# Kernel tuning notes

Measured on AMD Instinct MI355X. Metric: run time of the kernel, lower is better.

The kernel has to match this reference:

```python
import jax, jax.numpy as jnp
import numpy as np
from jax import lax

N_CLASS = 21
K_ED = 5
ALPHA = 0.1
BN_EPS = 1e-5


def _conv(x, w):
    # NCHW conv, stride 1, SAME padding
    return lax.conv_general_dilated(x, w, (1, 1), 'SAME',
                                    dimension_numbers=('NCHW', 'OIHW', 'NCHW'))


def _bn(x, g, b, m, v):
    # inference-mode BatchNorm2d with running stats
    scale = (g * lax.rsqrt(v + BN_EPS))[None, :, None, None]
    return (x - m[None, :, None, None]) * scale + b[None, :, None, None]


def _maxpool(x, k):
    return lax.reduce_window(x, -jnp.inf, lax.max, (1, 1, k, k), (1, 1, 1, 1), 'SAME')


def setup_inputs() -> dict:
    key = jax.random.key(0)
    ks = jax.random.split(key, 12)
    N, F, H, W, C = 8, 512, 96, 96, N_CLASS
    feature = jax.random.normal(ks[0], (N, F, H, W), jnp.float32)
    global_pred = jax.random.normal(ks[1], (N, C, H, W), jnp.float32)
    conv1_w = jax.random.normal(ks[2], (256, F, 3, 3), jnp.float32) * 0.02
    bn1_g = jnp.ones((256,), jnp.float32)
    bn1_b = jnp.zeros((256,), jnp.float32)
    bn1_m = jax.random.normal(ks[3], (256,), jnp.float32) * 0.1
    bn1_v = jax.random.uniform(ks[4], (256,), jnp.float32, 0.5, 1.5)
    conv2_w = jax.random.normal(ks[5], (128, 256, 3, 3), jnp.float32) * 0.02
    bn2_g = jnp.ones((128,), jnp.float32)
    bn2_b = jnp.zeros((128,), jnp.float32)
    bn2_m = jax.random.normal(ks[6], (128,), jnp.float32) * 0.1
    bn2_v = jax.random.uniform(ks[7], (128,), jnp.float32, 0.5, 1.5)
    conv3_w = jax.random.normal(ks[8], (C, 128, 1, 1), jnp.float32) * 0.02
    conv3_b = jnp.zeros((C,), jnp.float32)
    return dict(feature=feature, global_pred=global_pred,
                conv1_w=conv1_w, bn1_g=bn1_g, bn1_b=bn1_b, bn1_m=bn1_m, bn1_v=bn1_v,
                conv2_w=conv2_w, bn2_g=bn2_g, bn2_b=bn2_b, bn2_m=bn2_m, bn2_v=bn2_v,
                conv3_w=conv3_w, conv3_b=conv3_b)


def reference(feature, global_pred, conv1_w, bn1_g, bn1_b, bn1_m, bn1_v,
              conv2_w, bn2_g, bn2_b, bn2_m, bn2_v, conv3_w, conv3_b):
    N, F, H, W = feature.shape
    # hard labels -> one-hot [N, C, H, W]
    lbl = jnp.argmax(global_pred, axis=1)
    onehot = jnp.transpose(jax.nn.one_hot(lbl, N_CLASS, dtype=feature.dtype), (0, 3, 1, 2))
    # binary morphology: dilation = max-pool, erosion = -max-pool(-x)
    d = _maxpool(onehot, K_ED)
    e = -_maxpool(-onehot, K_ED)
    transition = jnp.sum(d - e, axis=1, keepdims=True)
    transition = jnp.where(transition >= 1.0, 1.0, transition)  # [N,1,H,W]
    tfeat = feature * transition
    # per-class masked mean over ALL H*W pixels (faithful to .mean(dim=2))
    objs = jnp.einsum('nfhw,nchw->ncf', feature, e) / (H * W)  # [N,C,F]
    # cdist(p=2) between transition-feature pixels and class prototypes
    x = tfeat.reshape(N, F, H * W).transpose(0, 2, 1)  # [N,HW,F]
    x2 = jnp.sum(x * x, axis=-1, keepdims=True)
    o2 = jnp.sum(objs * objs, axis=-1)
    d2 = jnp.maximum(x2 + o2[:, None, :] - 2.0 * jnp.einsum('npf,ncf->npc', x, objs), 0.0)
    cd = jnp.where(d2 > 0, jnp.sqrt(jnp.where(d2 > 0, d2, 1.0)), 0.0)  # safe sqrt
    dist = 1.0 - jax.nn.softmax(cd, axis=-1)  # [N,HW,C]
    obj_feat = jnp.einsum('npc,ncf->nfp', dist, objs).reshape(N, F, H, W)
    fusion = (feature * (1.0 - transition)
              + feature * transition * ALPHA
              + obj_feat * transition * (1.0 - ALPHA))
    # fusion_predictor: convBNReLU -> bilinear x2 -> convBNReLU -> 1x1 conv
    h = jax.nn.relu(_bn(_conv(fusion, conv1_w), bn1_g, bn1_b, bn1_m, bn1_v))
    h = jax.image.resize(h, (N, 256, 2 * H, 2 * W), method='bilinear')
    h = jax.nn.relu(_bn(_conv(h, conv2_w), bn2_g, bn2_b, bn2_m, bn2_v))
    logits = _conv(h, conv3_w) + conv3_b[None, :, None, None]
    # eval mode: softmax over classes
    return jax.nn.softmax(logits, axis=1)
```

## Files before the change

### kernel.cpp

```cpp
#include <hip/hip_runtime.h>
#include <cstdint>
#include <cstddef>

typedef __attribute__((ext_vector_type(4))) float f32x4;
typedef __attribute__((ext_vector_type(8))) short short8;

__device__ __forceinline__ float bf2f(unsigned short u) {
  union { unsigned int i; float f; } x; x.i = ((unsigned int)u) << 16; return x.f;
}
__device__ __forceinline__ unsigned short f2bf(float f) {
  union { float f; unsigned int i; } x; x.f = f;
  unsigned int r = x.i + 0x7fffu + ((x.i >> 16) & 1u);
  return (unsigned short)(r >> 16);
}
__device__ __forceinline__ void gload16(unsigned short* lds, const unsigned short* g) {
  __builtin_amdgcn_global_load_lds(
      (const __attribute__((address_space(1))) unsigned int*)g,
      (__attribute__((address_space(3))) unsigned int*)lds, 16, 0, 0);
}

__global__ void k_prepbn(const float* __restrict__ g1, const float* __restrict__ b1,
                         const float* __restrict__ m1, const float* __restrict__ v1,
                         const float* __restrict__ g2, const float* __restrict__ b2,
                         const float* __restrict__ m2, const float* __restrict__ v2,
                         float* __restrict__ s1, float* __restrict__ bb1,
                         float* __restrict__ s2, float* __restrict__ bb2) {
  int i = threadIdx.x;
  if (i < 256) { float s = g1[i] * rsqrtf(v1[i] + 1e-5f); s1[i] = s; bb1[i] = b1[i] - m1[i] * s; }
  if (i < 128) { float s = g2[i] * rsqrtf(v2[i] + 1e-5f); s2[i] = s; bb2[i] = b2[i] - m2[i] * s; }
}

__global__ void k_prepw1(const float* __restrict__ w, unsigned short* __restrict__ wt) {
  int i = blockIdx.x * 256 + threadIdx.x;
  int o = i / 4608, k = i - o * 4608;
  int cblk = k / 288, r = k - cblk * 288;
  int t = r >> 5, cl = r & 31;
  int ci = cblk * 32 + cl;
  int ty = t / 3, tx = t - ty * 3;
  wt[i] = f2bf(w[((o * 512 + ci) * 3 + ty) * 3 + tx]);
}
__global__ void k_prepw2(const float* __restrict__ w, unsigned short* __restrict__ wt) {
  int i = blockIdx.x * 256 + threadIdx.x;
  int o = i / 2304, k = i - o * 2304;
  int cblk = k / 288, r = k - cblk * 288;
  int t = r >> 5, cl = r & 31;
  int ci = cblk * 32 + cl;
  int ty = t / 3, tx = t - ty * 3;
  wt[i] = f2bf(w[((o * 256 + ci) * 3 + ty) * 3 + tx]);
}
__global__ void k_prepw3(const float* __restrict__ w3, unsigned short* __restrict__ w3b) {
  int i = blockIdx.x * 256 + threadIdx.x;
  int c = i >> 7, k = i & 127;
  w3b[i] = (c < 21) ? f2bf(w3[c * 128 + k]) : (unsigned short)0;
}

template <int HP, int WP, int C>
__global__ void k_border(unsigned short* __restrict__ p) {
  const int B = 2 * WP + 2 * (HP - 2);
  const int total = 8 * B * (C / 8);
  int i = blockIdx.x * 256 + threadIdx.x;
  if (i >= total) return;
  const int cg = i % (C / 8);
  int b = i / (C / 8);
  const int n = b / B; b -= n * B;
  int y, x;
  if (b < WP) { y = 0; x = b; }
  else if (b < 2 * WP) { y = HP - 1; x = b - WP; }
  else { int r = b - 2 * WP; y = 1 + (r >> 1); x = (r & 1) ? (WP - 1) : 0; }
  short8 z = {0, 0, 0, 0, 0, 0, 0, 0};
  *(short8*)&p[(((long)n * HP + y) * WP + x) * C + cg * 8] = z;
}

__global__ __launch_bounds__(256)
void k_featT(const float* __restrict__ feat, unsigned short* __restrict__ featT) {
  const int g = blockIdx.x * 256 + threadIdx.x;
  const int n = g / 9216, p = g - n * 9216;
  const int fg0 = blockIdx.y * 16;
  const float* src = feat + (long)n * 512 * 9216 + p;
  unsigned short* dst = featT + ((long)n * 9216 + p) * 512;
  for (int fg = fg0; fg < fg0 + 16; fg++) {
    short8 o;
    #pragma unroll
    for (int j = 0; j < 8; j++) o[j] = (short)f2bf(src[(long)(fg * 8 + j) * 9216]);
    *(short8*)&dst[fg * 8] = o;
  }
}

__global__ void k_labels(const float* __restrict__ gp, signed char* __restrict__ lab) {
  int p = blockIdx.x * 256 + threadIdx.x;
  int n = p / 9216, q = p - n * 9216;
  const float* g = gp + (long)n * 21 * 9216 + q;
  float best = g[0]; int bi = 0;
  #pragma unroll
  for (int c = 1; c < 21; c++) {
    float v = g[(long)c * 9216];
    if (v > best) { best = v; bi = c; }
  }
  lab[p] = (signed char)bi;
}

__global__ void k_em(const signed char* __restrict__ lab, signed char* __restrict__ em) {
  int p = blockIdx.x * 256 + threadIdx.x;
  int n = p / 9216, q = p - n * 9216, y = q / 96, x = q - y * 96;
  const signed char* L = lab + n * 9216;
  signed char l0 = L[q];
  bool uni = true;
  for (int dy = -2; dy <= 2; dy++) {
    int yy = y + dy; if (yy < 0 || yy > 95) continue;
    for (int dx = -2; dx <= 2; dx++) {
      int xx = x + dx; if (xx < 0 || xx > 95) continue;
      uni = uni && (L[yy * 96 + xx] == l0);
    }
  }
  em[p] = uni ? l0 : (signed char)-1;
}

__global__ __launch_bounds__(256)
void k_objsT(const unsigned short* __restrict__ featT, const signed char* __restrict__ em,
             float* __restrict__ objs) {
  __shared__ float part[21 * 512];
  __shared__ signed char emL[256];
  __shared__ int pres[21];
  const int b = blockIdx.x;
  const int n = b / 36;
  const int px0 = (b - n * 36) * 256;
  const int tid = threadIdx.x;
  for (int i = tid; i < 21 * 512; i += 256) part[i] = 0.f;
  if (tid < 21) pres[tid] = 0;
  emL[tid] = em[n * 9216 + px0 + tid];
  __syncthreads();
  const unsigned short* base = featT + ((long)n * 9216 + px0) * 512 + tid * 2;
  for (int px = 0; px < 256; px++) {
    const int c0 = emL[px];
    if (c0 >= 0) {
      if (tid == 0) pres[c0] = 1;
      unsigned int v = *(const unsigned int*)&base[(long)px * 512];
      atomicAdd(&part[c0 * 512 + tid * 2], bf2f((unsigned short)(v & 0xffff)));
      atomicAdd(&part[c0 * 512 + tid * 2 + 1], bf2f((unsigned short)(v >> 16)));
    }
  }
  __syncthreads();
  for (int i = tid; i < 21 * 512; i += 256) {
    const int c = i >> 9;
    if (pres[c]) atomicAdd(&objs[(long)n * 21 * 512 + i], part[i] * (1.0f / 9216.0f));
  }
}

__global__ void k_o2(const float* __restrict__ objs, float* __restrict__ o2) {
  int nc = blockIdx.x;
  int lane = threadIdx.x;
  const float* o = objs + (long)nc * 512;
  float s = 0.f;
  for (int f = lane; f < 512; f += 64) { float v = o[f]; s += v * v; }
  #pragma unroll
  for (int off = 32; off; off >>= 1) s += __shfl_down(s, off);
  if (lane == 0) o2[nc] = s;
}

__global__ void k_objsbf(const float* __restrict__ objs, unsigned short* __restrict__ oc) {
  int i = blockIdx.x * 256 + threadIdx.x;
  int n = i / (32 * 512); int r = i - n * 32 * 512;
  int c = r >> 9, f = r & 511;
  oc[i] = (c < 21) ? f2bf(objs[((long)n * 21 + c) * 512 + f]) : (unsigned short)0;
}

__global__ __launch_bounds__(256)
void k_dist_mfma(const unsigned short* __restrict__ featT,
                 const unsigned short* __restrict__ objs_c,
                 const float* __restrict__ o2, float* __restrict__ dist) {
  const int n = blockIdx.y;
  const int w = threadIdx.x >> 6, lane = threadIdx.x & 63;
  const int lrow = lane & 15, kg = lane >> 4;
  const int px = blockIdx.x * 64 + w * 16 + lrow;
  const unsigned short* fb = featT + ((long)n * 9216 + px) * 512 + kg * 8;
  const unsigned short* a0p = objs_c + ((long)n * 32 + lrow) * 512 + kg * 8;
  const unsigned short* a1p = a0p + 16 * 512;
  f32x4 acc0 = {0.f, 0.f, 0.f, 0.f}, acc1 = {0.f, 0.f, 0.f, 0.f};
  float x2 = 0.f;
  #pragma unroll
  for (int s = 0; s < 16; s++) {
    const short8 b = *(const short8*)&fb[s * 32];
    const short8 a0 = *(const short8*)&a0p[s * 32];
    const short8 a1 = *(const short8*)&a1p[s * 32];
    acc0 = __builtin_amdgcn_mfma_f32_16x16x32_bf16(a0, b, acc0, 0, 0, 0);
    acc1 = __builtin_amdgcn_mfma_f32_16x16x32_bf16(a1, b, acc1, 0, 0, 0);
    #pragma unroll
    for (int j = 0; j < 8; j++) { float v = bf2f((unsigned short)b[j]); x2 += v * v; }
  }
  x2 += __shfl_xor(x2, 16); x2 += __shfl_xor(x2, 32);
  float cd[8], mx = -1e30f;
  #pragma unroll
  for (int r = 0; r < 4; r++) {
    const int c = kg * 4 + r;
    float d2 = x2 + o2[n * 21 + c] - 2.f * acc0[r];
    cd[r] = sqrtf(fmaxf(d2, 0.f)); mx = fmaxf(mx, cd[r]);
  }
  #pragma unroll
  for (int r = 0; r < 4; r++) {
    const int c = 16 + kg * 4 + r;
    if (c < 21) {
      float d2 = x2 + o2[n * 21 + c] - 2.f * acc1[r];
      cd[4 + r] = sqrtf(fmaxf(d2, 0.f)); mx = fmaxf(mx, cd[4 + r]);
    } else cd[4 + r] = -1e30f;
  }
  mx = fmaxf(mx, __shfl_xor(mx, 16)); mx = fmaxf(mx, __shfl_xor(mx, 32));
  float sum = 0.f;
  #pragma unroll
  for (int k = 0; k < 8; k++) {
    cd[k] = (cd[k] > -1e29f) ? __expf(cd[k] - mx) : 0.f;
    sum += cd[k];
  }
  sum += __shfl_xor(sum, 16); sum += __shfl_xor(sum, 32);
  const float inv = 1.f / sum;
  #pragma unroll
  for (int r = 0; r < 4; r++)
    dist[((long)n * 21 + kg * 4 + r) * 9216 + px] = 1.f - cd[r] * inv;
  #pragma unroll
  for (int r = 0; r < 4; r++) {
    const int c = 16 + kg * 4 + r;
    if (c < 21) dist[((long)n * 21 + c) * 9216 + px] = 1.f - cd[4 + r] * inv;
  }
}

__global__ __launch_bounds__(256)
void k_fusion(const unsigned short* __restrict__ featT, const signed char* __restrict__ em,
              const float* __restrict__ dist, const float* __restrict__ objs,
              unsigned short* __restrict__ fuP) {
  __shared__ float ob[21 * 512];
  __shared__ float dl[64][21];
  __shared__ signed char eml[64];
  const int blk = blockIdx.x;
  const int n = blk / 144;
  const int p0 = (blk - n * 144) * 64;
  const int tid = threadIdx.x;
  for (int i = tid; i < 21 * 512; i += 256) ob[i] = objs[(long)n * 21 * 512 + i];
  for (int i = tid; i < 64 * 21; i += 256) {
    int px = i & 63, c = i >> 6;
    dl[px][c] = dist[((long)n * 21 + c) * 9216 + p0 + px];
  }
  if (tid < 64) eml[tid] = em[n * 9216 + p0 + tid];
  __syncthreads();
  const int px = tid & 63;
  const int fg = (tid >> 6) * 8;
  const int q = p0 + px;
  const int y = q / 96, x = q - y * 96;
  unsigned short* dst = fuP + (((long)n * 98 + y + 1) * 98 + (x + 1)) * 512;
  const bool t = eml[px] < 0;
  const unsigned short* srcT = featT + ((long)n * 9216 + q) * 512;
  for (int f0 = 0; f0 < 512; f0 += 32) {
    short8 o;
    const short8 fvv = *(const short8*)&srcT[f0 + fg];
    #pragma unroll
    for (int j = 0; j < 8; j++) {
      const int f = f0 + fg + j;
      float fv = bf2f((unsigned short)fvv[j]);
      if (t) {
        float of = 0.f;
        #pragma unroll
        for (int c = 0; c < 21; c++) of += dl[px][c] * ob[c * 512 + f];
        fv = 0.1f * fv + 0.9f * of;
      }
      o[j] = (short)f2bf(fv);
    }
    *(short8*)&dst[fg] = o;
    dst += 32;
  }
}

template <int CIN, int NK>
__global__ __launch_bounds__(256)
void conv3x3_gemm(const unsigned short* __restrict__ inP,
                  const unsigned short* __restrict__ wT,
                  const float* __restrict__ scale, const float* __restrict__ bias,
                  unsigned short* __restrict__ out,
                  int Hout, int Wout, int Hp, int Wp, int COUT, int nbN) {
  __shared__ unsigned short ldsA[3][4096];
  __shared__ unsigned short ldsB[3][4096];
  const int tid = threadIdx.x;
  const int chunk = gridDim.x >> 3;
  const int bid = (blockIdx.x & 7) * chunk + (blockIdx.x >> 3);
  const int mb = bid / nbN, nb = bid - mb * nbN;
  const int bm0 = mb * 128, bn0 = nb * 128;
  const int KT = 9 * CIN;
  const int HWo = Hout * Wout;

  const int rA = tid >> 2;
  const int ch8 = (((tid & 3) ^ ((tid >> 3) & 3)) * 8);
  const int m0 = bm0 + rA, m1 = m0 + 64;
  const int n0 = m0 / HWo; const int q0 = m0 - n0 * HWo;
  const int y0 = q0 / Wout, x0 = q0 - y0 * Wout;
  const int n1 = m1 / HWo; const int q1 = m1 - n1 * HWo;
  const int y1 = q1 / Wout, x1 = q1 - y1 * Wout;
  const unsigned short* gA0 = inP + ((long)(n0 * Hp + y0) * Wp + x0) * CIN + ch8;
  const unsigned short* gA1 = inP + ((long)(n1 * Hp + y1) * Wp + x1) * CIN + ch8;
  const unsigned short* gB0 = wT + (long)(bn0 + rA) * KT + ch8;
  const unsigned short* gB1 = wT + (long)(bn0 + rA + 64) * KT + ch8;

  const int lane = tid & 63;
  const int wv = tid >> 6;
  const int wr = wv >> 1, wc = wv & 1;
  const int lrow = lane & 15, kg = lane >> 4;
  const int arow = wr * 64 + lrow;
  const int aoff = arow * 32 + (kg ^ ((arow >> 1) & 3)) * 8;
  const int brow = wc * 64 + lrow;
  const int boff = brow * 32 + (kg ^ ((brow >> 1) & 3)) * 8;

  f32x4 acc[4][4];
  const f32x4 zero = {0.f, 0.f, 0.f, 0.f};
  #pragma unroll
  for (int i = 0; i < 4; i++)
    #pragma unroll
    for (int j = 0; j < 4; j++) acc[i][j] = zero;

  auto stage = [&](int b, int s) {
    const int cblk = s / 9;
    const int t = s - cblk * 9;
    const int ty = t / 3, tx = t - ty * 3;
    const long offA = (long)(ty * Wp + tx) * CIN + cblk * 32;
    gload16(&ldsA[b][tid * 8], gA0 + offA);
    gload16(&ldsA[b][2048 + tid * 8], gA1 + offA);
    const long k0 = (long)s * 32;
    gload16(&ldsB[b][tid * 8], gB0 + k0);
    gload16(&ldsB[b][2048 + tid * 8], gB1 + k0);
  };

  auto kstep = [&](int rd) {
    const unsigned short* A = ldsA[rd];
    const unsigned short* B = ldsB[rd];
    short8 af[4], bfr[4];
    #pragma unroll
    for (int i = 0; i < 4; i++) af[i] = *(const short8*)&A[aoff + i * 512];
    #pragma unroll
    for (int j = 0; j < 4; j++) bfr[j] = *(const short8*)&B[boff + j * 512];
    __builtin_amdgcn_s_setprio(1);
    #pragma unroll
    for (int i = 0; i < 4; i++)
      #pragma unroll
      for (int j = 0; j < 4; j++)
        acc[i][j] = __builtin_amdgcn_mfma_f32_16x16x32_bf16(af[i], bfr[j], acc[i][j], 0, 0, 0);
    __builtin_amdgcn_s_setprio(0);
  };

  stage(0, 0);
  stage(1, 1);
  int rd = 0;
  for (int s = 0; s < NK; ++s) {
    if (s < NK - 1)
      asm volatile("s_waitcnt vmcnt(6)" ::: "memory");
    else
      asm volatile("s_waitcnt vmcnt(0)" ::: "memory");
    __builtin_amdgcn_s_barrier();
    asm volatile("" ::: "memory");
    kstep(rd);
    if (s + 2 < NK) stage((rd + 2 >= 3) ? rd - 1 : rd + 2, s + 2);
    rd = (rd == 2) ? 0 : rd + 1;
  }

  #pragma unroll
  for (int i = 0; i < 4; i++) {
    const int row = bm0 + wr * 64 + i * 16 + kg * 4;
    #pragma unroll
    for (int j = 0; j < 4; j++) {
      const int col = bn0 + wc * 64 + j * 16 + lrow;
      const float sc = scale[col], bi = bias[col];
      #pragma unroll
      for (int r = 0; r < 4; r++) {
        float v = acc[i][j][r] * sc + bi;
        v = v > 0.f ? v : 0.f;
        out[(long)(row + r) * COUT + col] = f2bf(v);
      }
    }
  }
}

__global__ void k_upsample(const unsigned short* __restrict__ h1,
                           unsigned short* __restrict__ h2P) {
  const int idx = blockIdx.x * 256 + threadIdx.x;
  const int c8 = (idx & 31) * 8;
  const int p = idx >> 5;
  const int n = p / 36864; const int rr = p - n * 36864;
  const int Y = rr / 192, X = rr - Y * 192;
  const int ky = Y >> 1, kx = X >> 1;
  int yA, yB, xA, xB; float wyA, wyB, wxA, wxB;
  if ((Y & 1) == 0) { yA = ky > 0 ? ky - 1 : 0; yB = ky; wyA = 0.25f; wyB = 0.75f; }
  else { yA = ky; yB = ky < 95 ? ky + 1 : 95; wyA = 0.75f; wyB = 0.25f; }
  if ((X & 1) == 0) { xA = kx > 0 ? kx - 1 : 0; xB = kx; wxA = 0.25f; wxB = 0.75f; }
  else { xA = kx; xB = kx < 95 ? kx + 1 : 95; wxA = 0.75f; wxB = 0.25f; }
  const unsigned short* hb = h1 + (long)n * 96 * 96 * 256 + c8;
  const short8 vaa = *(const short8*)&hb[((long)yA * 96 + xA) * 256];
  const short8 vab = *(const short8*)&hb[((long)yA * 96 + xB) * 256];
  const short8 vba = *(const short8*)&hb[((long)yB * 96 + xA) * 256];
  const short8 vbb = *(const short8*)&hb[((long)yB * 96 + xB) * 256];
  short8 o;
  #pragma unroll
  for (int j = 0; j < 8; j++) {
    float v = wyA * (wxA * bf2f((unsigned short)vaa[j]) + wxB * bf2f((unsigned short)vab[j])) +
              wyB * (wxA * bf2f((unsigned short)vba[j]) + wxB * bf2f((unsigned short)vbb[j]));
    o[j] = (short)f2bf(v);
  }
  *(short8*)&h2P[(((long)n * 194 + Y + 1) * 194 + X + 1) * 256 + c8] = o;
}

__global__ __launch_bounds__(256)
void k_conv3_mfma(const unsigned short* __restrict__ h3,
                  const unsigned short* __restrict__ w3b,
                  const float* __restrict__ b3, float* __restrict__ out) {
  const int w = threadIdx.x >> 6, lane = threadIdx.x & 63;
  const int lrow = lane & 15, kg = lane >> 4;
  const long m = (long)blockIdx.x * 64 + w * 16 + lrow;
  const unsigned short* bp = h3 + m * 128 + kg * 8;
  const unsigned short* a0p = w3b + lrow * 128 + kg * 8;
  const unsigned short* a1p = a0p + 16 * 128;
  f32x4 acc0 = {0.f, 0.f, 0.f, 0.f}, acc1 = {0.f, 0.f, 0.f, 0.f};
  #pragma unroll
  for (int s = 0; s < 4; s++) {
    const short8 b = *(const short8*)&bp[s * 32];
    const short8 a0 = *(const short8*)&a0p[s * 32];
    const short8 a1 = *(const short8*)&a1p[s * 32];
    acc0 = __builtin_amdgcn_mfma_f32_16x16x32_bf16(a0, b, acc0, 0, 0, 0);
    acc1 = __builtin_amdgcn_mfma_f32_16x16x32_bf16(a1, b, acc1, 0, 0, 0);
  }
  float lg[8], mx = -1e30f;
  #pragma unroll
  for (int r = 0; r < 4; r++) {
    lg[r] = acc0[r] + b3[kg * 4 + r];
    mx = fmaxf(mx, lg[r]);
  }
  #pragma unroll
  for (int r = 0; r < 4; r++) {
    const int c = 16 + kg * 4 + r;
    if (c < 21) { lg[4 + r] = acc1[r] + b3[c]; mx = fmaxf(mx, lg[4 + r]); }
    else lg[4 + r] = -1e30f;
  }
  mx = fmaxf(mx, __shfl_xor(mx, 16)); mx = fmaxf(mx, __shfl_xor(mx, 32));
  float sum = 0.f;
  #pragma unroll
  for (int k = 0; k < 8; k++) {
    lg[k] = (lg[k] > -1e29f) ? __expf(lg[k] - mx) : 0.f;
    sum += lg[k];
  }
  sum += __shfl_xor(sum, 16); sum += __shfl_xor(sum, 32);
  const float inv = 1.f / sum;
  const int n = (int)(m / 36864);
  const int q = (int)(m - (long)n * 36864);
  #pragma unroll
  for (int r = 0; r < 4; r++)
    out[((long)n * 21 + kg * 4 + r) * 36864 + q] = lg[r] * inv;
  #pragma unroll
  for (int r = 0; r < 4; r++) {
    const int c = 16 + kg * 4 + r;
    if (c < 21) out[((long)n * 21 + c) * 36864 + q] = lg[4 + r] * inv;
  }
}

extern "C" void kernel_launch(void* const* d_in, const int* in_sizes, int n_in,
                              void* d_out, int out_size, void* d_ws, size_t ws_size,
                              hipStream_t stream) {
  const float* feature = (const float*)d_in[0];
  const float* gp = (const float*)d_in[1];
  const float* w1 = (const float*)d_in[2];
  const float* g1 = (const float*)d_in[3];
  const float* b1 = (const float*)d_in[4];
  const float* m1 = (const float*)d_in[5];
  const float* v1 = (const float*)d_in[6];
  const float* w2 = (const float*)d_in[7];
  const float* g2 = (const float*)d_in[8];
  const float* b2 = (const float*)d_in[9];
  const float* m2 = (const float*)d_in[10];
  const float* v2 = (const float*)d_in[11];
  const float* w3 = (const float*)d_in[12];
  const float* b3 = (const float*)d_in[13];
  float* out = (float*)d_out;

  char* ws = (char*)d_ws;
  size_t off = 0;
  auto alloc = [&](size_t bytes) -> void* {
    void* p = ws + off;
    off += (bytes + 255) & ~(size_t)255;
    return p;
  };
  signed char* lab = (signed char*)alloc(73728);
  signed char* em = (signed char*)alloc(73728);
  float* objs = (float*)alloc(8 * 21 * 512 * 4);
  float* o2 = (float*)alloc(168 * 4);
  unsigned short* objs_c = (unsigned short*)alloc((size_t)8 * 32 * 512 * 2);
  float* dist = (float*)alloc((size_t)8 * 21 * 9216 * 4);
  unsigned short* w1t = (unsigned short*)alloc((size_t)256 * 4608 * 2);
  unsigned short* w2t = (unsigned short*)alloc((size_t)128 * 2304 * 2);
  unsigned short* w3b = (unsigned short*)alloc((size_t)32 * 128 * 2);
  float* s1 = (float*)alloc(256 * 4);
  float* bb1 = (float*)alloc(256 * 4);
  float* s2 = (float*)alloc(128 * 4);
  float* bb2 = (float*)alloc(128 * 4);
  const size_t fuP_bytes = (size_t)8 * 98 * 98 * 512 * 2;
  unsigned short* fuP = (unsigned short*)alloc(fuP_bytes);
  const size_t h1_bytes = (size_t)8 * 96 * 96 * 256 * 2;
  unsigned short* h1 = (unsigned short*)alloc(h1_bytes);
  const size_t h2P_bytes = (size_t)8 * 194 * 194 * 256 * 2;
  unsigned short* h2P = (unsigned short*)alloc(h2P_bytes);
  unsigned short* h3 = fuP;
  unsigned short* featT = h2P;

  if (off > ws_size) return;

  k_prepbn<<<1, 256, 0, stream>>>(g1, b1, m1, v1, g2, b2, m2, v2, s1, bb1, s2, bb2);
  k_prepw1<<<4608, 256, 0, stream>>>(w1, w1t);
  k_prepw2<<<1152, 256, 0, stream>>>(w2, w2t);
  k_prepw3<<<16, 256, 0, stream>>>(w3, w3b);

  k_border<98, 98, 512><<<777, 256, 0, stream>>>(fuP);
  hipMemsetAsync(objs, 0, 8 * 21 * 512 * 4, stream);

  k_labels<<<288, 256, 0, stream>>>(gp, lab);
  k_em<<<288, 256, 0, stream>>>(lab, em);
  k_featT<<<dim3(288, 4), 256, 0, stream>>>(feature, featT);
  k_objsT<<<288, 256, 0, stream>>>(featT, em, objs);
  k_o2<<<168, 64, 0, stream>>>(objs, o2);
  k_objsbf<<<512, 256, 0, stream>>>(objs, objs_c);
  k_dist_mfma<<<dim3(144, 8), 256, 0, stream>>>(featT, objs_c, o2, dist);
  k_fusion<<<1152, 256, 0, stream>>>(featT, em, dist, objs, fuP);

  conv3x3_gemm<512, 144><<<1152, 256, 0, stream>>>(fuP, w1t, s1, bb1, h1,
                                                   96, 96, 98, 98, 256, 2);
  k_border<194, 194, 256><<<772, 256, 0, stream>>>(h2P);
  k_upsample<<<36864, 256, 0, stream>>>(h1, h2P);
  conv3x3_gemm<256, 72><<<2304, 256, 0, stream>>>(h2P, w2t, s2, bb2, h3,
                                                  192, 192, 194, 194, 128, 1);
  k_conv3_mfma<<<4608, 256, 0, stream>>>(h3, w3b, b3, out);
}
```

Before: 796.5 us.

## Fuse conv2 with 1x1 conv3 and softmax; deepen conv1 pipeline to 4 stages

The second 3x3 conv GEMM now keeps its BN+ReLU output tile in shared memory and immediately applies the 1x1 classifier conv via MFMA plus softmax. This removes the h3 intermediate write/read and a separate kernel launch. Separately, the generic conv GEMM (now used only for conv1) moves from triple to quadruple LDS buffering, with three stages in flight and adjusted vmcnt waits. The deeper buffering raises LDS use per block and may reduce occupancy.

```diff
diff --git a/kernel.cpp b/kernel.cpp
--- a/kernel.cpp
+++ b/kernel.cpp
@@ -274,8 +274,8 @@
                   const float* __restrict__ scale, const float* __restrict__ bias,
                   unsigned short* __restrict__ out,
                   int Hout, int Wout, int Hp, int Wp, int COUT, int nbN) {
-  __shared__ unsigned short ldsA[3][4096];
-  __shared__ unsigned short ldsB[3][4096];
+  __shared__ unsigned short ldsA[4][4096];
+  __shared__ unsigned short ldsB[4][4096];
   const int tid = threadIdx.x;
   const int chunk = gridDim.x >> 3;
   const int bid = (blockIdx.x & 7) * chunk + (blockIdx.x >> 3);
@@ -343,17 +343,18 @@
 
   stage(0, 0);
   stage(1, 1);
-  int rd = 0;
+  stage(2, 2);
   for (int s = 0; s < NK; ++s) {
-    if (s < NK - 1)
-      asm volatile("s_waitcnt vmcnt(6)" ::: "memory");
+    if (s <= NK - 3)
+      asm volatile("s_waitcnt vmcnt(8)" ::: "memory");
+    else if (s == NK - 2)
+      asm volatile("s_waitcnt vmcnt(4)" ::: "memory");
     else
       asm volatile("s_waitcnt vmcnt(0)" ::: "memory");
     __builtin_amdgcn_s_barrier();
     asm volatile("" ::: "memory");
-    kstep(rd);
-    if (s + 2 < NK) stage((rd + 2 >= 3) ? rd - 1 : rd + 2, s + 2);
-    rd = (rd == 2) ? 0 : rd + 1;
+    kstep(s & 3);
+    if (s + 3 < NK) stage((s + 3) & 3, s + 3);
   }
 
   #pragma unroll
@@ -369,6 +370,165 @@
         v = v > 0.f ? v : 0.f;
         out[(long)(row + r) * COUT + col] = f2bf(v);
       }
+    }
+  }
+}
+
+__global__ __launch_bounds__(256)
+void conv2_fused(const unsigned short* __restrict__ inP,
+                 const unsigned short* __restrict__ wT,
+                 const float* __restrict__ scale, const float* __restrict__ bias,
+                 const unsigned short* __restrict__ w3b, const float* __restrict__ b3,
+                 float* __restrict__ out) {
+  constexpr int CIN = 256, NK = 72;
+  constexpr int Wout = 192, Hp = 194, Wp = 194;
+  constexpr int HWo = 192 * 192;
+  constexpr int KT = 9 * CIN;
+  __shared__ unsigned short pool[6 * 4096];
+  const int tid = threadIdx.x;
+  const int chunk = gridDim.x >> 3;
+  const int bid = (blockIdx.x & 7) * chunk + (blockIdx.x >> 3);
+  const int bm0 = bid * 128;
+
+  const int rA = tid >> 2;
+  const int ch8 = (((tid & 3) ^ ((tid >> 3) & 3)) * 8);
+  const int m0 = bm0 + rA, m1 = m0 + 64;
+  const int n0 = m0 / HWo; const int q0 = m0 - n0 * HWo;
+  const int y0 = q0 / Wout, x0 = q0 - y0 * Wout;
+  const int n1 = m1 / HWo; const int q1 = m1 - n1 * HWo;
+  const int y1 = q1 / Wout, x1 = q1 - y1 * Wout;
+  const unsigned short* gA0 = inP + ((long)(n0 * Hp + y0) * Wp + x0) * CIN + ch8;
+  const unsigned short* gA1 = inP + ((long)(n1 * Hp + y1) * Wp + x1) * CIN + ch8;
+  const unsigned short* gB0 = wT + (long)rA * KT + ch8;
+  const unsigned short* gB1 = wT + (long)(rA + 64) * KT + ch8;
+
+  const int lane = tid & 63;
+  const int wv = tid >> 6;
+  const int wr = wv >> 1, wc = wv & 1;
+  const int lrow = lane & 15, kg = lane >> 4;
+  const int arow = wr * 64 + lrow;
+  const int aoff = arow * 32 + (kg ^ ((arow >> 1) & 3)) * 8;
+  const int brow = wc * 64 + lrow;
+  const int boff = brow * 32 + (kg ^ ((brow >> 1) & 3)) * 8;
+
+  f32x4 acc[4][4];
+  const f32x4 zero = {0.f, 0.f, 0.f, 0.f};
+  #pragma unroll
+  for (int i = 0; i < 4; i++)
+    #pragma unroll
+    for (int j = 0; j < 4; j++) acc[i][j] = zero;
+
+  auto stage = [&](int b, int s) {
+    const int cblk = s / 9;
+    const int t = s - cblk * 9;
+    const int ty = t / 3, tx = t - ty * 3;
+    const long offA = (long)(ty * Wp + tx) * CIN + cblk * 32;
+    gload16(&pool[b * 4096 + tid * 8], gA0 + offA);
+    gload16(&pool[b * 4096 + 2048 + tid * 8], gA1 + offA);
+    const long k0 = (long)s * 32;
+    gload16(&pool[12288 + b * 4096 + tid * 8], gB0 + k0);
+    gload16(&pool[12288 + b * 4096 + 2048 + tid * 8], gB1 + k0);
+  };
+
+  auto kstep = [&](int rd) {
+    const unsigned short* A = &pool[rd * 4096];
+    const unsigned short* B = &pool[12288 + rd * 4096];
+    short8 af[4], bfr[4];
+    #pragma unroll
+    for (int i = 0; i < 4; i++) af[i] = *(const short8*)&A[aoff + i * 512];
+    #pragma unroll
+    for (int j = 0; j < 4; j++) bfr[j] = *(const short8*)&B[boff + j * 512];
+    __builtin_amdgcn_s_setprio(1);
+    #pragma unroll
+    for (int i = 0; i < 4; i++)
+      #pragma unroll
+      for (int j = 0; j < 4; j++)
+        acc[i][j] = __builtin_amdgcn_mfma_f32_16x16x32_bf16(af[i], bfr[j], acc[i][j], 0, 0, 0);
+    __builtin_amdgcn_s_setprio(0);
+  };
+
+  stage(0, 0);
+  stage(1, 1);
+  int rd = 0;
+  for (int s = 0; s < NK; ++s) {
+    if (s < NK - 1)
+      asm volatile("s_waitcnt vmcnt(4)" ::: "memory");
+    else
+      asm volatile("s_waitcnt vmcnt(0)" ::: "memory");
+    __builtin_amdgcn_s_barrier();
+    asm volatile("" ::: "memory");
+    kstep(rd);
+    if (s + 2 < NK) stage((rd + 2 >= 3) ? rd - 1 : rd + 2, s + 2);
+    rd = (rd == 2) ? 0 : rd + 1;
+  }
+
+  asm volatile("s_waitcnt lgkmcnt(0)" ::: "memory");
+  __builtin_amdgcn_s_barrier();
+  asm volatile("" ::: "memory");
+  #pragma unroll
+  for (int j = 0; j < 4; j++) {
+    const int ch = wc * 64 + j * 16 + lrow;
+    const float sc = scale[ch], bi = bias[ch];
+    #pragma unroll
+    for (int i = 0; i < 4; i++) {
+      const int pxb = wr * 64 + i * 16 + kg * 4;
+      #pragma unroll
+      for (int r = 0; r < 4; r++) {
+        const int px = pxb + r;
+        float v = acc[i][j][r] * sc + bi;
+        v = v > 0.f ? v : 0.f;
+        pool[px * 128 + (ch ^ ((px & 7) << 3))] = f2bf(v);
+      }
+    }
+  }
+  asm volatile("s_waitcnt lgkmcnt(0)" ::: "memory");
+  __builtin_amdgcn_s_barrier();
+  asm volatile("" ::: "memory");
+
+  #pragma unroll
+  for (int g = 0; g < 2; g++) {
+    const int px = wv * 32 + g * 16 + lrow;
+    f32x4 acc0 = {0.f, 0.f, 0.f, 0.f}, acc1 = {0.f, 0.f, 0.f, 0.f};
+    #pragma unroll
+    for (int s = 0; s < 4; s++) {
+      const int ch0 = s * 32 + kg * 8;
+      const short8 b = *(const short8*)&pool[px * 128 + (ch0 ^ ((px & 7) << 3))];
+      const short8 a0 = *(const short8*)&w3b[lrow * 128 + ch0];
+      const short8 a1 = *(const short8*)&w3b[(16 + lrow) * 128 + ch0];
+      acc0 = __builtin_amdgcn_mfma_f32_16x16x32_bf16(a0, b, acc0, 0, 0, 0);
+      acc1 = __builtin_amdgcn_mfma_f32_16x16x32_bf16(a1, b, acc1, 0, 0, 0);
+    }
+    float lg[8], mx = -1e30f;
+    #pragma unroll
+    for (int r = 0; r < 4; r++) {
+      lg[r] = acc0[r] + b3[kg * 4 + r];
+      mx = fmaxf(mx, lg[r]);
+    }
+    #pragma unroll
+    for (int r = 0; r < 4; r++) {
+      const int c = 16 + kg * 4 + r;
+      if (c < 21) { lg[4 + r] = acc1[r] + b3[c]; mx = fmaxf(mx, lg[4 + r]); }
+      else lg[4 + r] = -1e30f;
+    }
+    mx = fmaxf(mx, __shfl_xor(mx, 16)); mx = fmaxf(mx, __shfl_xor(mx, 32));
+    float sum = 0.f;
+    #pragma unroll
+    for (int k = 0; k < 8; k++) {
+      lg[k] = (lg[k] > -1e29f) ? __expf(lg[k] - mx) : 0.f;
+      sum += lg[k];
+    }
+    sum += __shfl_xor(sum, 16); sum += __shfl_xor(sum, 32);
+    const float inv = 1.f / sum;
+    const int m = bm0 + px;
+    const int n = m / HWo;
+    const int q = m - n * HWo;
+    #pragma unroll
+    for (int r = 0; r < 4; r++)
+      out[((long)n * 21 + kg * 4 + r) * (long)HWo + q] = lg[r] * inv;
+    #pragma unroll
+    for (int r = 0; r < 4; r++) {
+      const int c = 16 + kg * 4 + r;
+      if (c < 21) out[((long)n * 21 + c) * (long)HWo + q] = lg[4 + r] * inv;
     }
   }
 }
@@ -399,58 +559,6 @@
     o[j] = (short)f2bf(v);
   }
   *(short8*)&h2P[(((long)n * 194 + Y + 1) * 194 + X + 1) * 256 + c8] = o;
-}
-
-__global__ __launch_bounds__(256)
-void k_conv3_mfma(const unsigned short* __restrict__ h3,
-                  const unsigned short* __restrict__ w3b,
-                  const float* __restrict__ b3, float* __restrict__ out) {
-  const int w = threadIdx.x >> 6, lane = threadIdx.x & 63;
-  const int lrow = lane & 15, kg = lane >> 4;
-  const long m = (long)blockIdx.x * 64 + w * 16 + lrow;
-  const unsigned short* bp = h3 + m * 128 + kg * 8;
-  const unsigned short* a0p = w3b + lrow * 128 + kg * 8;
-  const unsigned short* a1p = a0p + 16 * 128;
-  f32x4 acc0 = {0.f, 0.f, 0.f, 0.f}, acc1 = {0.f, 0.f, 0.f, 0.f};
-  #pragma unroll
-  for (int s = 0; s < 4; s++) {
-    const short8 b = *(const short8*)&bp[s * 32];
-    const short8 a0 = *(const short8*)&a0p[s * 32];
-    const short8 a1 = *(const short8*)&a1p[s * 32];
-    acc0 = __builtin_amdgcn_mfma_f32_16x16x32_bf16(a0, b, acc0, 0, 0, 0);
-    acc1 = __builtin_amdgcn_mfma_f32_16x16x32_bf16(a1, b, acc1, 0, 0, 0);
-  }
-  float lg[8], mx = -1e30f;
-  #pragma unroll
-  for (int r = 0; r < 4; r++) {
-    lg[r] = acc0[r] + b3[kg * 4 + r];
-    mx = fmaxf(mx, lg[r]);
-  }
-  #pragma unroll
-  for (int r = 0; r < 4; r++) {
-    const int c = 16 + kg * 4 + r;
-    if (c < 21) { lg[4 + r] = acc1[r] + b3[c]; mx = fmaxf(mx, lg[4 + r]); }
-    else lg[4 + r] = -1e30f;
-  }
-  mx = fmaxf(mx, __shfl_xor(mx, 16)); mx = fmaxf(mx, __shfl_xor(mx, 32));
-  float sum = 0.f;
-  #pragma unroll
-  for (int k = 0; k < 8; k++) {
-    lg[k] = (lg[k] > -1e29f) ? __expf(lg[k] - mx) : 0.f;
-    sum += lg[k];
-  }
-  sum += __shfl_xor(sum, 16); sum += __shfl_xor(sum, 32);
-  const float inv = 1.f / sum;
-  const int n = (int)(m / 36864);
-  const int q = (int)(m - (long)n * 36864);
-  #pragma unroll
-  for (int r = 0; r < 4; r++)
-    out[((long)n * 21 + kg * 4 + r) * 36864 + q] = lg[r] * inv;
-  #pragma unroll
-  for (int r = 0; r < 4; r++) {
-    const int c = 16 + kg * 4 + r;
-    if (c < 21) out[((long)n * 21 + c) * 36864 + q] = lg[4 + r] * inv;
-  }
 }
 
 extern "C" void kernel_launch(void* const* d_in, const int* in_sizes, int n_in,
@@ -498,7 +606,6 @@
   unsigned short* h1 = (unsigned short*)alloc(h1_bytes);
   const size_t h2P_bytes = (size_t)8 * 194 * 194 * 256 * 2;
   unsigned short* h2P = (unsigned short*)alloc(h2P_bytes);
-  unsigned short* h3 = fuP;
   unsigned short* featT = h2P;
 
   if (off > ws_size) return;
@@ -524,7 +631,5 @@
                                                    96, 96, 98, 98, 256, 2);
   k_border<194, 194, 256><<<772, 256, 0, stream>>>(h2P);
   k_upsample<<<36864, 256, 0, stream>>>(h1, h2P);
-  conv3x3_gemm<256, 72><<<2304, 256, 0, stream>>>(h2P, w2t, s2, bb2, h3,
-                                                  192, 192, 194, 194, 128, 1);
-  k_conv3_mfma<<<4608, 256, 0, stream>>>(h3, w3b, b3, out);
-}
+  conv2_fused<<<2304, 256, 0, stream>>>(h2P, w2t, s2, bb2, w3b, b3, out);
+}
```

Result: no change. 800.5 us (+0.5%).
